# Optimization experiments

Measured on AMD Instinct MI355X. Metric: run time of the kernel, lower is better.

## Reference

```python
import jax, jax.numpy as jnp
import numpy as np

D = 128  # feature_dim

def setup_inputs() -> dict:
    key = jax.random.key(0)
    ks = jax.random.split(key, 10)
    B, Sq, Skv = 32, 2048, 2048
    scale = 1.0 / np.sqrt(D)
    inp = {
        'smiles_features': jax.random.normal(ks[0], (B, Skv, D), jnp.float32),
        'image_features': jax.random.normal(ks[1], (B, Sq, D), jnp.float32),
        'Wv': jax.random.normal(ks[2], (D, D), jnp.float32) * scale,
        'bv': jnp.zeros((D,), jnp.float32),
        'Wk': jax.random.normal(ks[3], (D, D), jnp.float32) * scale,
        'bk': jnp.zeros((D,), jnp.float32),
        'Wq': jax.random.normal(ks[4], (D, D), jnp.float32) * scale,
        'bq': jnp.zeros((D,), jnp.float32),
        'Wd': jax.random.normal(ks[5], (D, D), jnp.float32) * scale,
        'bd': jnp.zeros((D,), jnp.float32),
    }
    return inp

def reference(smiles_features, image_features, Wv, bv, Wk, bk, Wq, bq, Wd, bd):
    # Linear layers: y = x @ W^T + b (torch convention)
    V = smiles_features @ Wv.T + bv          # [B, Skv, D]
    K = smiles_features @ Wk.T + bk          # [B, Skv, D]
    Q = image_features @ Wq.T + bq           # [B, Sq, D]
    # energy = Q K^T / sqrt(128) (hard-coded 128 in original)
    energy = jnp.einsum('bqd,bkd->bqk', Q, K) / jnp.sqrt(jnp.float32(128.0))
    attention = jax.nn.softmax(energy, axis=-1)
    fusion = jnp.einsum('bqk,bkd->bqd', attention, V)
    output = fusion @ Wd.T + bd
    return output
```

## Files before the change

### kernel.cpp

```cpp
#include <hip/hip_runtime.h>
#include <hip/hip_bf16.h>

typedef __attribute__((ext_vector_type(4))) float f32x4;
typedef __attribute__((ext_vector_type(16))) float f32x16;
typedef __attribute__((ext_vector_type(8))) short bf16x8;
typedef __attribute__((ext_vector_type(4))) unsigned int uint4v;
typedef __attribute__((ext_vector_type(2))) unsigned int uint2v;

#define MFMA16(a, b, c) __builtin_amdgcn_mfma_f32_16x16x32_bf16(a, b, c, 0, 0, 0)
#define MFMA32(a, b, c) __builtin_amdgcn_mfma_f32_32x32x16_bf16(a, b, c, 0, 0, 0)

__device__ __forceinline__ unsigned short f2bf(float f) {
  union { float f; unsigned u; } v; v.f = f;
  unsigned r = v.u + 0x7fffu + ((v.u >> 16) & 1u);
  return (unsigned short)(r >> 16);
}
__device__ __forceinline__ unsigned pack2(float a, float b) {
  union { __hip_bfloat162 h2; unsigned u; } cv;
  cv.h2 = __hip_bfloat162(__float2bfloat16(a), __float2bfloat16(b));
  return cv.u;
}

__device__ __forceinline__ void swap32(unsigned a, unsigned b, int hi,
                                       unsigned& ox, unsigned& oy) {
#if __has_builtin(__builtin_amdgcn_permlane32_swap)
  uint2v r = __builtin_amdgcn_permlane32_swap(a, b, false, false);
  ox = r[0]; oy = r[1];
#else
  unsigned sb = __shfl_xor(b, 32);
  unsigned sa = __shfl_xor(a, 32);
  ox = hi ? sb : a;
  oy = hi ? b : sa;
#endif
}

template<bool IN_F32, int OUT_MODE>
__global__ __launch_bounds__(256)
void proj_kernel(const void* __restrict__ xin, const float* __restrict__ W,
                 const float* __restrict__ bias, void* __restrict__ yout,
                 float scale)
{
  __shared__ __align__(16) unsigned short Ws[128][136];
  __shared__ __align__(16) unsigned short Xs[64][136];
  const int t = threadIdx.x;
  const int wid = t >> 6;
  const int lane = t & 63;
  const int ln = lane & 15, g = lane >> 4;
  const long row0 = (long)blockIdx.x * 64;

  float bz[8];
#pragma unroll
  for (int tt = 0; tt < 8; ++tt) bz[tt] = bias[tt * 16 + ln];

#pragma unroll
  for (int i = 0; i < 16; ++i) {
    int idx = (i * 256 + t) * 4;
    int r = idx >> 7, c = idx & 127;
    const float4 w4 = *reinterpret_cast<const float4*>(W + idx);
    ushort4 wb;
    wb.x = f2bf(w4.x); wb.y = f2bf(w4.y); wb.z = f2bf(w4.z); wb.w = f2bf(w4.w);
    *reinterpret_cast<ushort4*>(&Ws[r][c]) = wb;
  }
  if (IN_F32) {
    const float* x = (const float*)xin;
#pragma unroll
    for (int i = 0; i < 8; ++i) {
      int idx = (i * 256 + t) * 4;
      int r = idx >> 7, c = idx & 127;
      const float4 x4 = *reinterpret_cast<const float4*>(x + row0 * 128 + idx);
      ushort4 xb;
      xb.x = f2bf(x4.x); xb.y = f2bf(x4.y); xb.z = f2bf(x4.z); xb.w = f2bf(x4.w);
      *reinterpret_cast<ushort4*>(&Xs[r][c]) = xb;
    }
  } else {
    const unsigned short* x = (const unsigned short*)xin;
#pragma unroll
    for (int i = 0; i < 4; ++i) {
      int idx = (i * 256 + t) * 8;
      int r = idx >> 7, c = idx & 127;
      *reinterpret_cast<uint4v*>(&Xs[r][c]) =
          *reinterpret_cast<const uint4v*>(x + row0 * 128 + idx);
    }
  }
  __syncthreads();

  f32x4 acc[8];
#pragma unroll
  for (int tt = 0; tt < 8; ++tt) acc[tt] = (f32x4){0.f, 0.f, 0.f, 0.f};

#pragma unroll
  for (int c = 0; c < 4; ++c) {
    bf16x8 af = *reinterpret_cast<const bf16x8*>(&Xs[wid * 16 + ln][c * 32 + g * 8]);
#pragma unroll
    for (int tt = 0; tt < 8; ++tt) {
      bf16x8 bfr = *reinterpret_cast<const bf16x8*>(&Ws[tt * 16 + ln][c * 32 + g * 8]);
      acc[tt] = MFMA16(af, bfr, acc[tt]);
    }
  }

#pragma unroll
  for (int tt = 0; tt < 8; ++tt) {
#pragma unroll
    for (int r = 0; r < 4; ++r) {
      long row = row0 + wid * 16 + g * 4 + r;
      int col = tt * 16 + ln;
      float val = (acc[tt][r] + bz[tt]) * scale;
      if (OUT_MODE == 2) {
        ((float*)yout)[row * 128 + col] = val;
      } else {
        ((unsigned short*)yout)[row * 128 + col] = f2bf(val);
      }
    }
  }
}

__global__ __launch_bounds__(256)
void proj_qkv_kernel(const float* __restrict__ image,
                     const float* __restrict__ Wq, const float* __restrict__ bq,
                     float qscale,
                     const float* __restrict__ smiles,
                     const float* __restrict__ Wk, const float* __restrict__ bk,
                     const float* __restrict__ Wv, const float* __restrict__ bv,
                     unsigned short* __restrict__ Qout,
                     unsigned short* __restrict__ Kout,
                     unsigned short* __restrict__ Vout)
{
  __shared__ __align__(16) unsigned short Ws[128][136];
  __shared__ __align__(16) unsigned short Xs[64][136];
  const int t = threadIdx.x;
  const int wid = t >> 6;
  const int lane = t & 63;
  const int ln = lane & 15, g = lane >> 4;
  const bool isQ = blockIdx.x < 1024;
  const long row0 = (long)(isQ ? blockIdx.x : blockIdx.x - 1024) * 64;
  const float* x = isQ ? image : smiles;

#pragma unroll
  for (int i = 0; i < 8; ++i) {
    int idx = (i * 256 + t) * 4;
    int r = idx >> 7, c = idx & 127;
    const float4 x4 = *reinterpret_cast<const float4*>(x + row0 * 128 + idx);
    ushort4 xb;
    xb.x = f2bf(x4.x); xb.y = f2bf(x4.y); xb.z = f2bf(x4.z); xb.w = f2bf(x4.w);
    *reinterpret_cast<ushort4*>(&Xs[r][c]) = xb;
  }

  const float* W1 = isQ ? Wq : Wk;
  const float* b1 = isQ ? bq : bk;
  float bz[8];
#pragma unroll
  for (int tt = 0; tt < 8; ++tt) bz[tt] = b1[tt * 16 + ln];

#pragma unroll
  for (int i = 0; i < 16; ++i) {
    int idx = (i * 256 + t) * 4;
    int r = idx >> 7, c = idx & 127;
    const float4 w4 = *reinterpret_cast<const float4*>(W1 + idx);
    ushort4 wb;
    wb.x = f2bf(w4.x); wb.y = f2bf(w4.y); wb.z = f2bf(w4.z); wb.w = f2bf(w4.w);
    *reinterpret_cast<ushort4*>(&Ws[r][c]) = wb;
  }
  __syncthreads();

  f32x4 acc[8];
#pragma unroll
  for (int tt = 0; tt < 8; ++tt) acc[tt] = (f32x4){0.f, 0.f, 0.f, 0.f};
#pragma unroll
  for (int c = 0; c < 4; ++c) {
    bf16x8 af = *reinterpret_cast<const bf16x8*>(&Xs[wid * 16 + ln][c * 32 + g * 8]);
#pragma unroll
    for (int tt = 0; tt < 8; ++tt) {
      bf16x8 bfr = *reinterpret_cast<const bf16x8*>(&Ws[tt * 16 + ln][c * 32 + g * 8]);
      acc[tt] = MFMA16(af, bfr, acc[tt]);
    }
  }

  if (isQ) {
#pragma unroll
    for (int tt = 0; tt < 8; ++tt)
#pragma unroll
      for (int r = 0; r < 4; ++r) {
        long row = row0 + wid * 16 + g * 4 + r;
        Qout[row * 128 + tt * 16 + ln] = f2bf((acc[tt][r] + bz[tt]) * qscale);
      }
    return;
  }

#pragma unroll
  for (int tt = 0; tt < 8; ++tt)
#pragma unroll
    for (int r = 0; r < 4; ++r) {
      long row = row0 + wid * 16 + g * 4 + r;
      Kout[row * 128 + tt * 16 + ln] = f2bf(acc[tt][r] + bz[tt]);
    }

  __syncthreads();
#pragma unroll
  for (int i = 0; i < 16; ++i) {
    int idx = (i * 256 + t) * 4;
    int r = idx >> 7, c = idx & 127;
    const float4 w4 = *reinterpret_cast<const float4*>(Wv + idx);
    ushort4 wb;
    wb.x = f2bf(w4.x); wb.y = f2bf(w4.y); wb.z = f2bf(w4.z); wb.w = f2bf(w4.w);
    *reinterpret_cast<ushort4*>(&Ws[r][c]) = wb;
  }
  __syncthreads();

  float bzv[8];
#pragma unroll
  for (int tt = 0; tt < 8; ++tt) bzv[tt] = bv[tt * 16 + ln];
#pragma unroll
  for (int tt = 0; tt < 8; ++tt) acc[tt] = (f32x4){0.f, 0.f, 0.f, 0.f};
#pragma unroll
  for (int c = 0; c < 4; ++c) {
    bf16x8 af = *reinterpret_cast<const bf16x8*>(&Xs[wid * 16 + ln][c * 32 + g * 8]);
#pragma unroll
    for (int tt = 0; tt < 8; ++tt) {
      bf16x8 bfr = *reinterpret_cast<const bf16x8*>(&Ws[tt * 16 + ln][c * 32 + g * 8]);
      acc[tt] = MFMA16(af, bfr, acc[tt]);
    }
  }
#pragma unroll
  for (int tt = 0; tt < 8; ++tt)
#pragma unroll
    for (int r = 0; r < 4; ++r) {
      long row = row0 + wid * 16 + g * 4 + r;
      long bb = row >> 11, rr = row & 2047;
      Vout[(bb * 128 + tt * 16 + ln) * 2048 + rr] = f2bf(acc[tt][r] + bzv[tt]);
    }
}

__global__ __launch_bounds__(256)
void attn_kernel(const unsigned short* __restrict__ Qg,
                 const unsigned short* __restrict__ Kg,
                 const unsigned short* __restrict__ Vtg,
                 unsigned short* __restrict__ Fg)
{
  __shared__ __align__(16) unsigned short Ks[2][32][136];
  __shared__ __align__(16) unsigned short Vs[2][128][40];

  const int t = threadIdx.x;
  const int lane = t & 63;
  const int q = lane & 31;
  const int hi = lane >> 5;
  const int wid = t >> 6;

  const int gbid = blockIdx.x;
  const int k_ = gbid >> 3, r_ = gbid & 7;
  const int b = r_ + 8 * (k_ >> 4);
  const int j = k_ & 15;
  const int q0 = j * 128 + wid * 32;

  const unsigned short* Qb = Qg + (long)b * 2048 * 128;
  const unsigned short* Kb = Kg + (long)b * 2048 * 128;
  const unsigned short* Vb = Vtg + (long)b * 128 * 2048;

  const int kr = t >> 4, kc = (t & 15) * 8;
  const int vc = t >> 2, ko = (t & 3) * 8;

  bf16x8 qf[8];
#pragma unroll
  for (int c = 0; c < 8; ++c)
    qf[c] = *reinterpret_cast<const bf16x8*>(
        Qb + (long)(q0 + q) * 128 + c * 16 + hi * 8);

  f32x16 o[4];
#pragma unroll
  for (int dc = 0; dc < 4; ++dc)
#pragma unroll
    for (int r = 0; r < 16; ++r) o[dc][r] = 0.f;
  float mrun = -1e30f;
  float lrun = 0.f;

  uint4v kreg0 = *reinterpret_cast<const uint4v*>(Kb + (long)kr * 128 + kc);
  uint4v kreg1 = *reinterpret_cast<const uint4v*>(Kb + (long)(kr + 16) * 128 + kc);
  uint4v vreg0 = *reinterpret_cast<const uint4v*>(Vb + (long)vc * 2048 + ko);
  uint4v vreg1 = *reinterpret_cast<const uint4v*>(Vb + (long)(vc + 64) * 2048 + ko);
  *reinterpret_cast<uint4v*>(&Ks[0][kr][kc]) = kreg0;
  *reinterpret_cast<uint4v*>(&Ks[0][kr + 16][kc]) = kreg1;
  *reinterpret_cast<uint4v*>(&Vs[0][vc][ko]) = vreg0;
  *reinterpret_cast<uint4v*>(&Vs[0][vc + 64][ko]) = vreg1;
  kreg0 = *reinterpret_cast<const uint4v*>(Kb + (long)(32 + kr) * 128 + kc);
  kreg1 = *reinterpret_cast<const uint4v*>(Kb + (long)(32 + kr + 16) * 128 + kc);
  vreg0 = *reinterpret_cast<const uint4v*>(Vb + (long)vc * 2048 + 32 + ko);
  vreg1 = *reinterpret_cast<const uint4v*>(Vb + (long)(vc + 64) * 2048 + 32 + ko);
  __syncthreads();

  for (int kt = 0; kt < 64; ++kt) {
    const int cur = kt & 1;

    if (kt < 63) {
      const int nb = cur ^ 1;
      *reinterpret_cast<uint4v*>(&Ks[nb][kr][kc]) = kreg0;
      *reinterpret_cast<uint4v*>(&Ks[nb][kr + 16][kc]) = kreg1;
      *reinterpret_cast<uint4v*>(&Vs[nb][vc][ko]) = vreg0;
      *reinterpret_cast<uint4v*>(&Vs[nb][vc + 64][ko]) = vreg1;
      if (kt < 62) {
        const int nv0 = (kt + 2) * 32;
        kreg0 = *reinterpret_cast<const uint4v*>(Kb + (long)(nv0 + kr) * 128 + kc);
        kreg1 = *reinterpret_cast<const uint4v*>(Kb + (long)(nv0 + kr + 16) * 128 + kc);
        vreg0 = *reinterpret_cast<const uint4v*>(Vb + (long)vc * 2048 + nv0 + ko);
        vreg1 = *reinterpret_cast<const uint4v*>(Vb + (long)(vc + 64) * 2048 + nv0 + ko);
      }
    }

    f32x16 st;
#pragma unroll
    for (int r = 0; r < 16; ++r) st[r] = 0.f;
    __builtin_amdgcn_s_setprio(1);
#pragma unroll
    for (int c = 0; c < 8; ++c) {
      bf16x8 kf = *reinterpret_cast<const bf16x8*>(&Ks[cur][q][c * 16 + hi * 8]);
      st = MFMA32(kf, qf[c], st);
    }
    __builtin_amdgcn_s_setprio(0);

    float tm = st[0];
#pragma unroll
    for (int r = 1; r < 16; ++r) tm = fmaxf(tm, st[r]);
    tm = fmaxf(tm, __shfl_xor(tm, 32));

    float mcur = mrun;
    if (!__all(tm <= mcur + 8.0f)) {
      float mnew = fmaxf(mcur, tm);
      float al = __builtin_amdgcn_exp2f(mcur - mnew);
      mrun = mnew;
      mcur = mnew;
      lrun *= al;
#pragma unroll
      for (int r = 0; r < 16; ++r) {
        float ar = __shfl(al, (r & 3) + 8 * (r >> 2) + 4 * hi);
#pragma unroll
        for (int dc = 0; dc < 4; ++dc) o[dc][r] *= ar;
      }
    }

    unsigned pk[8];
    float s[8];
#pragma unroll
    for (int j2 = 0; j2 < 8; ++j2) {
      float pa_ = __builtin_amdgcn_exp2f(st[2 * j2] - mcur);
      float pb_ = __builtin_amdgcn_exp2f(st[2 * j2 + 1] - mcur);
      s[j2] = pa_ + pb_;
      pk[j2] = pack2(pa_, pb_);
    }
#pragma unroll
    for (int j2 = 0; j2 < 4; ++j2) s[j2] += s[j2 + 4];
    lrun += (s[0] + s[1]) + (s[2] + s[3]);

    union { unsigned u[4]; bf16x8 v; } pa0, pa1;
    swap32(pk[0], pk[2], hi, pa0.u[0], pa0.u[2]);
    swap32(pk[1], pk[3], hi, pa0.u[1], pa0.u[3]);
    swap32(pk[4], pk[6], hi, pa1.u[0], pa1.u[2]);
    swap32(pk[5], pk[7], hi, pa1.u[1], pa1.u[3]);

    __builtin_amdgcn_s_setprio(1);
#pragma unroll
    for (int dc = 0; dc < 4; ++dc) {
      bf16x8 vf0 = *reinterpret_cast<const bf16x8*>(&Vs[cur][dc * 32 + q][hi * 8]);
      bf16x8 vf1 = *reinterpret_cast<const bf16x8*>(&Vs[cur][dc * 32 + q][16 + hi * 8]);
      o[dc] = MFMA32(pa0.v, vf0, o[dc]);
      o[dc] = MFMA32(pa1.v, vf1, o[dc]);
    }
    __builtin_amdgcn_s_setprio(0);

    __syncthreads();
  }

  float ltot = lrun + __shfl_xor(lrun, 32);
  float inv = 1.f / ltot;
#pragma unroll
  for (int r = 0; r < 16; ++r) {
    const int qr = (r & 3) + 8 * (r >> 2) + 4 * hi;
    float invr = __shfl(inv, qr);
    long row = (long)b * 2048 + q0 + qr;
#pragma unroll
    for (int dc = 0; dc < 4; ++dc)
      Fg[row * 128 + dc * 32 + q] = f2bf(o[dc][r] * invr);
  }
}

extern "C" void kernel_launch(void* const* d_in, const int* in_sizes, int n_in,
                              void* d_out, int out_size, void* d_ws, size_t ws_size,
                              hipStream_t stream)
{
  (void)in_sizes; (void)n_in; (void)out_size; (void)ws_size;
  const float* smiles = (const float*)d_in[0];
  const float* image  = (const float*)d_in[1];
  const float* Wv = (const float*)d_in[2]; const float* bv = (const float*)d_in[3];
  const float* Wk = (const float*)d_in[4]; const float* bk = (const float*)d_in[5];
  const float* Wq = (const float*)d_in[6]; const float* bq = (const float*)d_in[7];
  const float* Wd = (const float*)d_in[8]; const float* bd = (const float*)d_in[9];

  unsigned short* Qw = (unsigned short*)d_ws;
  unsigned short* Kw = Qw + 8388608;
  unsigned short* Vw = Kw + 8388608;
  unsigned short* Fw = Vw + 8388608;

  const float qscale = 1.4426950408889634f * 0.08838834764831845f;

  dim3 blk(256);
  proj_qkv_kernel<<<dim3(2048), blk, 0, stream>>>(image, Wq, bq, qscale,
                                                  smiles, Wk, bk, Wv, bv,
                                                  Qw, Kw, Vw);
  attn_kernel<<<dim3(512), blk, 0, stream>>>(Qw, Kw, Vw, Fw);
  proj_kernel<false, 2><<<dim3(1024), blk, 0, stream>>>(Fw, Wd, bd, (float*)d_out, 1.f);
}
```

Measured before the change: 126.0 us.

## Fuse output projection into attention kernel epilogue

The separate output-projection kernel is removed and its work moves into the end of the attention kernel. After attention, each wave writes its normalized bf16 output tile to shared memory, multiplies it by Wd (converted to bf16 in shared memory) with MFMA, adds the bias and writes fp32 directly. This drops one launch and the global round trip of the intermediate fusion tensor. The cost is a larger shared-memory footprint (68 KB), which may lower occupancy in the attention loop, plus per-block reloading of Wd.

```diff
diff --git a/kernel.cpp b/kernel.cpp
--- a/kernel.cpp
+++ b/kernel.cpp
@@ -32,86 +32,6 @@
   ox = hi ? sb : a;
   oy = hi ? b : sa;
 #endif
-}
-
-template<bool IN_F32, int OUT_MODE>
-__global__ __launch_bounds__(256)
-void proj_kernel(const void* __restrict__ xin, const float* __restrict__ W,
-                 const float* __restrict__ bias, void* __restrict__ yout,
-                 float scale)
-{
-  __shared__ __align__(16) unsigned short Ws[128][136];
-  __shared__ __align__(16) unsigned short Xs[64][136];
-  const int t = threadIdx.x;
-  const int wid = t >> 6;
-  const int lane = t & 63;
-  const int ln = lane & 15, g = lane >> 4;
-  const long row0 = (long)blockIdx.x * 64;
-
-  float bz[8];
-#pragma unroll
-  for (int tt = 0; tt < 8; ++tt) bz[tt] = bias[tt * 16 + ln];
-
-#pragma unroll
-  for (int i = 0; i < 16; ++i) {
-    int idx = (i * 256 + t) * 4;
-    int r = idx >> 7, c = idx & 127;
-    const float4 w4 = *reinterpret_cast<const float4*>(W + idx);
-    ushort4 wb;
-    wb.x = f2bf(w4.x); wb.y = f2bf(w4.y); wb.z = f2bf(w4.z); wb.w = f2bf(w4.w);
-    *reinterpret_cast<ushort4*>(&Ws[r][c]) = wb;
-  }
-  if (IN_F32) {
-    const float* x = (const float*)xin;
-#pragma unroll
-    for (int i = 0; i < 8; ++i) {
-      int idx = (i * 256 + t) * 4;
-      int r = idx >> 7, c = idx & 127;
-      const float4 x4 = *reinterpret_cast<const float4*>(x + row0 * 128 + idx);
-      ushort4 xb;
-      xb.x = f2bf(x4.x); xb.y = f2bf(x4.y); xb.z = f2bf(x4.z); xb.w = f2bf(x4.w);
-      *reinterpret_cast<ushort4*>(&Xs[r][c]) = xb;
-    }
-  } else {
-    const unsigned short* x = (const unsigned short*)xin;
-#pragma unroll
-    for (int i = 0; i < 4; ++i) {
-      int idx = (i * 256 + t) * 8;
-      int r = idx >> 7, c = idx & 127;
-      *reinterpret_cast<uint4v*>(&Xs[r][c]) =
-          *reinterpret_cast<const uint4v*>(x + row0 * 128 + idx);
-    }
-  }
-  __syncthreads();
-
-  f32x4 acc[8];
-#pragma unroll
-  for (int tt = 0; tt < 8; ++tt) acc[tt] = (f32x4){0.f, 0.f, 0.f, 0.f};
-
-#pragma unroll
-  for (int c = 0; c < 4; ++c) {
-    bf16x8 af = *reinterpret_cast<const bf16x8*>(&Xs[wid * 16 + ln][c * 32 + g * 8]);
-#pragma unroll
-    for (int tt = 0; tt < 8; ++tt) {
-      bf16x8 bfr = *reinterpret_cast<const bf16x8*>(&Ws[tt * 16 + ln][c * 32 + g * 8]);
-      acc[tt] = MFMA16(af, bfr, acc[tt]);
-    }
-  }
-
-#pragma unroll
-  for (int tt = 0; tt < 8; ++tt) {
-#pragma unroll
-    for (int r = 0; r < 4; ++r) {
-      long row = row0 + wid * 16 + g * 4 + r;
-      int col = tt * 16 + ln;
-      float val = (acc[tt][r] + bz[tt]) * scale;
-      if (OUT_MODE == 2) {
-        ((float*)yout)[row * 128 + col] = val;
-      } else {
-        ((unsigned short*)yout)[row * 128 + col] = f2bf(val);
-      }
-    }
-  }
 }
 
 __global__ __launch_bounds__(256)
@@ -234,10 +154,13 @@
 void attn_kernel(const unsigned short* __restrict__ Qg,
                  const unsigned short* __restrict__ Kg,
                  const unsigned short* __restrict__ Vtg,
-                 unsigned short* __restrict__ Fg)
+                 const float* __restrict__ Wd,
+                 const float* __restrict__ bd,
+                 float* __restrict__ Out)
 {
-  __shared__ __align__(16) unsigned short Ks[2][32][136];
-  __shared__ __align__(16) unsigned short Vs[2][128][40];
+  __shared__ __align__(16) unsigned char smem[69632];
+  auto Ks = reinterpret_cast<unsigned short (*)[32][136]>(smem);
+  auto Vs = reinterpret_cast<unsigned short (*)[128][40]>(smem + 17408);
 
   const int t = threadIdx.x;
   const int lane = t & 63;
@@ -367,16 +290,59 @@
     __syncthreads();
   }
 
+  auto Wds = reinterpret_cast<unsigned short (*)[136]>(smem);
+  auto Os  = reinterpret_cast<unsigned short (*)[136]>(smem + 34816 + wid * 8704);
+
+#pragma unroll
+  for (int i = 0; i < 16; ++i) {
+    int idx = (i * 256 + t) * 4;
+    int r = idx >> 7, c = idx & 127;
+    const float4 w4 = *reinterpret_cast<const float4*>(Wd + idx);
+    ushort4 wb;
+    wb.x = f2bf(w4.x); wb.y = f2bf(w4.y); wb.z = f2bf(w4.z); wb.w = f2bf(w4.w);
+    *reinterpret_cast<ushort4*>(&Wds[r][c]) = wb;
+  }
+
   float ltot = lrun + __shfl_xor(lrun, 32);
   float inv = 1.f / ltot;
 #pragma unroll
   for (int r = 0; r < 16; ++r) {
     const int qr = (r & 3) + 8 * (r >> 2) + 4 * hi;
     float invr = __shfl(inv, qr);
+#pragma unroll
+    for (int dc = 0; dc < 4; ++dc)
+      Os[qr][dc * 32 + q] = f2bf(o[dc][r] * invr);
+  }
+  __syncthreads();
+
+  f32x16 o2[4];
+#pragma unroll
+  for (int cc = 0; cc < 4; ++cc)
+#pragma unroll
+    for (int r = 0; r < 16; ++r) o2[cc][r] = 0.f;
+  __builtin_amdgcn_s_setprio(1);
+#pragma unroll
+  for (int c = 0; c < 8; ++c) {
+    bf16x8 af = *reinterpret_cast<const bf16x8*>(&Os[q][c * 16 + hi * 8]);
+#pragma unroll
+    for (int cc = 0; cc < 4; ++cc) {
+      bf16x8 bfr = *reinterpret_cast<const bf16x8*>(&Wds[cc * 32 + q][c * 16 + hi * 8]);
+      o2[cc] = MFMA32(af, bfr, o2[cc]);
+    }
+  }
+  __builtin_amdgcn_s_setprio(0);
+
+  float bdv[4];
+#pragma unroll
+  for (int cc = 0; cc < 4; ++cc) bdv[cc] = bd[cc * 32 + q];
+
+#pragma unroll
+  for (int r = 0; r < 16; ++r) {
+    const int qr = (r & 3) + 8 * (r >> 2) + 4 * hi;
     long row = (long)b * 2048 + q0 + qr;
 #pragma unroll
-    for (int dc = 0; dc < 4; ++dc)
-      Fg[row * 128 + dc * 32 + q] = f2bf(o[dc][r] * invr);
+    for (int cc = 0; cc < 4; ++cc)
+      Out[row * 128 + cc * 32 + q] = o2[cc][r] + bdv[cc];
   }
 }
 
@@ -395,7 +361,6 @@
   unsigned short* Qw = (unsigned short*)d_ws;
   unsigned short* Kw = Qw + 8388608;
   unsigned short* Vw = Kw + 8388608;
-  unsigned short* Fw = Vw + 8388608;
 
   const float qscale = 1.4426950408889634f * 0.08838834764831845f;
 
@@ -403,6 +368,5 @@
   proj_qkv_kernel<<<dim3(2048), blk, 0, stream>>>(image, Wq, bq, qscale,
                                                   smiles, Wk, bk, Wv, bv,
                                                   Qw, Kw, Vw);
-  attn_kernel<<<dim3(512), blk, 0, stream>>>(Qw, Kw, Vw, Fw);
-  proj_kernel<false, 2><<<dim3(1024), blk, 0, stream>>>(Fw, Wd, bd, (float*)d_out, 1.f);
-}
+  attn_kernel<<<dim3(512), blk, 0, stream>>>(Qw, Kw, Vw, Wd, bd, (float*)d_out);
+}
```

Result: faster. 118.6 us (-5.9%).
